# Performance work log

Measured on AMD Instinct MI355X. Metric: run time of the kernel, lower is better.

## Reference

```python
import jax, jax.numpy as jnp
import numpy as np

ALPHA = 0.2          # LeakyReLU negative slope
NEG_INF = -9e15      # mask value used by the original module


def setup_inputs() -> dict:
    key = jax.random.key(0)
    k1, k2, k3, k4 = jax.random.split(key, 4)
    N, F_IN, F_OUT = 8192, 512, 256
    inp = jax.random.normal(k1, (N, F_IN), dtype=jnp.float32)
    W = jax.random.normal(k2, (F_IN, F_OUT), dtype=jnp.float32) * (1.414 / np.sqrt(F_IN))
    a = jax.random.normal(k3, (2 * F_OUT, 1), dtype=jnp.float32) * (1.414 / np.sqrt(F_OUT))
    adj = jax.random.randint(k4, (N, N), 0, 2, dtype=jnp.int32)
    return {"input": inp, "W": W, "a": a, "adj": adj}


def reference(input, W, a, adj):
    # h: [N, F_out]
    h = input @ W
    F_out = h.shape[1]
    # Original builds a_input[i,j] = concat(h_i, h_j) then matmuls with a.
    # Equivalent: e_ij = leakyrelu(h_i . a[:F] + h_j . a[F:]) without the O(N^2 * 2F) tensor.
    a1 = a[:F_out, 0]   # [F_out]
    a2 = a[F_out:, 0]   # [F_out]
    s1 = h @ a1         # [N]
    s2 = h @ a2         # [N]
    e = jax.nn.leaky_relu(s1[:, None] + s2[None, :], negative_slope=ALPHA)  # [N, N]
    attention = jax.nn.softmax(jnp.where(adj > 0, e, NEG_INF), axis=1)       # [N, N]
    return attention @ h  # [N, F_out]
```

## Files before the change

kernel.cpp:

```cpp
#include <hip/hip_runtime.h>


typedef __attribute__((ext_vector_type(8))) short bf16x8;
typedef __attribute__((ext_vector_type(4))) float fx4;
typedef __attribute__((ext_vector_type(4))) int ix4;
typedef __attribute__((ext_vector_type(2))) unsigned int ux2;

#define NN 8192
#define FIN 512
#define FOUT 256
#define PS 136
#define AROWS 32

__device__ __forceinline__ unsigned short f2bf(float f) {
    unsigned int x = __float_as_uint(f);
    x += 0x7fffu + ((x >> 16) & 1u);
    return (unsigned short)(x >> 16);
}
__device__ __forceinline__ bf16x8 pack8(fx4 a, fx4 b) {
    bf16x8 r;
    r[0] = (short)f2bf(a[0]); r[1] = (short)f2bf(a[1]);
    r[2] = (short)f2bf(a[2]); r[3] = (short)f2bf(a[3]);
    r[4] = (short)f2bf(b[0]); r[5] = (short)f2bf(b[1]);
    r[6] = (short)f2bf(b[2]); r[7] = (short)f2bf(b[3]);
    return r;
}

__global__ void wt_kernel(const float* __restrict__ W,
                          unsigned short* __restrict__ WTt) {
    const int c = threadIdx.x;
    const int k = blockIdx.x;
    WTt[((size_t)(k >> 5) * 256 + c) * 32 + (k & 31)] = f2bf(W[k * FOUT + c]);
}

__global__ __launch_bounds__(256) void prep_kernel(
    const float* __restrict__ X,
    const unsigned short* __restrict__ WTt,
    const float* __restrict__ A,
    unsigned short* __restrict__ hTt,
    float* __restrict__ s1, float* __restrict__ s2)
{
    __shared__ float s1sh[4][16], s2sh[4][16];
    const int tid = threadIdx.x;

    const int w = tid >> 6, l = tid & 63, q = l >> 4, lr = l & 15;
    const int r0 = blockIdx.x * 16;
    const int cbase = w * 64;
    fx4 acc[4] = {};

    for (int kb = 0; kb < FIN; kb += 32) {
        const float* xp = X + (size_t)(r0 + lr) * FIN + kb + q * 8;
        bf16x8 a0 = pack8(*(const fx4*)xp, *(const fx4*)(xp + 4));
#pragma unroll
        for (int tc = 0; tc < 4; ++tc) {
            bf16x8 b = *(const bf16x8*)(WTt + ((size_t)(kb >> 5) * 256 + cbase + tc * 16 + lr) * 32 + q * 8);
            acc[tc] = __builtin_amdgcn_mfma_f32_16x16x32_bf16(a0, b, acc[tc], 0, 0, 0);
        }
    }

    const int jb = r0 >> 5, jo = (r0 & 31) + q * 4;
#pragma unroll
    for (int tc = 0; tc < 4; ++tc) {
        const int c = cbase + tc * 16 + lr;
        ux2 hp;
        hp.x = (unsigned)f2bf(acc[tc][0]) | ((unsigned)f2bf(acc[tc][1]) << 16);
        hp.y = (unsigned)f2bf(acc[tc][2]) | ((unsigned)f2bf(acc[tc][3]) << 16);
        *(ux2*)(hTt + ((size_t)jb * 256 + c) * 32 + jo) = hp;
    }

    float p1[4] = {}, p2[4] = {};
#pragma unroll
    for (int tc = 0; tc < 4; ++tc) {
        const int c = cbase + tc * 16 + lr;
        const float a1v = A[c], a2v = A[FOUT + c];
#pragma unroll
        for (int r = 0; r < 4; ++r) {
            p1[r] += acc[tc][r] * a1v;
            p2[r] += acc[tc][r] * a2v;
        }
    }
#pragma unroll
    for (int r = 0; r < 4; ++r) {
#pragma unroll
        for (int off = 1; off < 16; off <<= 1) {
            p1[r] += __shfl_xor(p1[r], off);
            p2[r] += __shfl_xor(p2[r], off);
        }
        if (lr == 0) { s1sh[w][q * 4 + r] = p1[r]; s2sh[w][q * 4 + r] = p2[r]; }
    }
    __syncthreads();
    if (tid < 16) {
        s1[r0 + tid] = s1sh[0][tid] + s1sh[1][tid] + s1sh[2][tid] + s1sh[3][tid];
        s2[r0 + tid] = s2sh[0][tid] + s2sh[1][tid] + s2sh[2][tid] + s2sh[3][tid];
    }
}

__global__ __launch_bounds__(512) void attn_kernel(
    const int* __restrict__ adj,
    const unsigned short* __restrict__ hTt,
    const float* __restrict__ s1,
    const float* __restrict__ s2,
    float* __restrict__ out)
{
    __shared__ unsigned short P[2][AROWS * PS];
    __shared__ float dsh[AROWS];

    const int tid = threadIdx.x;
    const int r0 = blockIdx.x * AROWS;

    const int prow = tid >> 4;
    const int pq = tid & 15;
    const float s1v = s1[r0 + prow];
    const int* arow = adj + (size_t)(r0 + prow) * NN + pq * 8;
    float denp = 0.f;

    const int w = tid >> 6, l = tid & 63, q = l >> 4, lr = l & 15;
    const int cbase = w * 32;
    fx4 acc[2][2] = {};

    struct LSet { ix4 v0, v1; fx4 s2a, s2b; };
    LSet LA, LB;
    bf16x8 B0[4][2], B1[4][2];

    auto loadP = [&](int kt, LSet& L) {
        const int* ap = arow + kt * 128;
        L.v0 = __builtin_nontemporal_load((const ix4*)ap);
        L.v1 = __builtin_nontemporal_load((const ix4*)(ap + 4));
        L.s2a = *(const fx4*)(s2 + kt * 128 + pq * 8);
        L.s2b = *(const fx4*)(s2 + kt * 128 + pq * 8 + 4);
    };
    auto calcP = [&](int b, const LSet& L) {
        bf16x8 pv;
#pragma unroll
        for (int j = 0; j < 8; ++j) {
            const int aj = (j < 4) ? L.v0[j] : L.v1[j - 4];
            const float s2j = (j < 4) ? L.s2a[j] : L.s2b[j - 4];
            float t = s1v + s2j;
            float e = fmaxf(t, 0.2f * t);
            e = fminf(e, 30.f);
            const float p = (aj != 0) ? __expf(e) : 0.f;
            denp += p;
            pv[j] = (short)f2bf(p);
        }
        *(bf16x8*)(&P[b][prow * PS + pq * 8]) = pv;
    };
    auto loadB = [&](int it, bf16x8 (&B)[4][2]) {
#pragma unroll
        for (int ks = 0; ks < 4; ++ks)
#pragma unroll
            for (int tc = 0; tc < 2; ++tc)
                B[ks][tc] = *(const bf16x8*)(hTt + ((size_t)(it * 4 + ks) * 256 + cbase + tc * 16 + lr) * 32 + q * 8);
    };

    auto ldsBarrier = [&]() {
        asm volatile("s_waitcnt lgkmcnt(0)" ::: "memory");
        __builtin_amdgcn_s_barrier();
    };

    const int ITERS = NN / 128;
    loadP(0, LA);
    calcP(0, LA);
    loadP(1, LA);
    loadB(0, B0);
    ldsBarrier();

    auto body = [&](int it, bf16x8 (&Bc)[4][2], bf16x8 (&Bn)[4][2],
                    LSet& Lc, LSet& Ln) {
        if (it + 1 < ITERS) loadB(it + 1, Bn);
        if (it + 2 < ITERS) loadP(it + 2, Ln);
        const unsigned short* Pb = P[it & 1];
        bf16x8 af0[4], af1[4];
#pragma unroll
        for (int ks = 0; ks < 4; ++ks) {
            af0[ks] = *(const bf16x8*)(Pb + lr * PS + ks * 32 + q * 8);
            af1[ks] = *(const bf16x8*)(Pb + (16 + lr) * PS + ks * 32 + q * 8);
        }
        __builtin_amdgcn_s_setprio(1);
#pragma unroll
        for (int ks = 0; ks < 4; ++ks)
#pragma unroll
            for (int tc = 0; tc < 2; ++tc) {
                acc[0][tc] = __builtin_amdgcn_mfma_f32_16x16x32_bf16(af0[ks], Bc[ks][tc], acc[0][tc], 0, 0, 0);
                acc[1][tc] = __builtin_amdgcn_mfma_f32_16x16x32_bf16(af1[ks], Bc[ks][tc], acc[1][tc], 0, 0, 0);
            }
        __builtin_amdgcn_s_setprio(0);
        if (it + 1 < ITERS) calcP((it + 1) & 1, Lc);
        ldsBarrier();
    };

    for (int it = 0; it < ITERS; it += 2) {
        body(it, B0, B1, LA, LB);
        body(it + 1, B1, B0, LB, LA);
    }

    float v = denp;
    v += __shfl_xor(v, 1);
    v += __shfl_xor(v, 2);
    v += __shfl_xor(v, 4);
    v += __shfl_xor(v, 8);
    if (pq == 0) dsh[prow] = v;
    __syncthreads();

#pragma unroll
    for (int mg = 0; mg < 2; ++mg) {
#pragma unroll
        for (int r = 0; r < 4; ++r) {
            const int row = mg * 16 + q * 4 + r;
            const float dinv = 1.0f / fmaxf(dsh[row], 1e-30f);
#pragma unroll
            for (int tc = 0; tc < 2; ++tc) {
                out[(size_t)(r0 + row) * FOUT + cbase + tc * 16 + lr] = acc[mg][tc][r] * dinv;
            }
        }
    }
}

extern "C" void kernel_launch(void* const* d_in, const int* in_sizes, int n_in,
                              void* d_out, int out_size, void* d_ws, size_t ws_size,
                              hipStream_t stream) {
    const float *X = nullptr, *W = nullptr, *A = nullptr;
    const int* adj = nullptr;
    for (int i = 0; i < n_in; ++i) {
        switch (in_sizes[i]) {
            case NN * FIN:   X = (const float*)d_in[i]; break;
            case FIN * FOUT: W = (const float*)d_in[i]; break;
            case 2 * FOUT:   A = (const float*)d_in[i]; break;
            case NN * NN:    adj = (const int*)d_in[i]; break;
        }
    }
    if (!X) X = (const float*)d_in[0];
    if (!W) W = (const float*)d_in[1];
    if (!A) A = (const float*)d_in[2];
    if (!adj) adj = (const int*)d_in[3];
    float* out = (float*)d_out;

    char* ws = (char*)d_ws;
    float* s1 = (float*)ws;
    float* s2 = (float*)(ws + 32768);
    unsigned short* WTt = (unsigned short*)(ws + 98304);
    unsigned short* hTt = (unsigned short*)(ws + 360448);

    wt_kernel<<<512, 256, 0, stream>>>(W, WTt);
    prep_kernel<<<512, 256, 0, stream>>>(X, WTt, A, hTt, s1, s2);
    attn_kernel<<<NN / AROWS, 512, 0, stream>>>(adj, hTt, s1, s2, out);
}
```

Measured before the change: 442.4 us.

## Retile attention kernel to 64 rows by 128 columns per block

The attention kernel now gives each block 64 rows and half of the output columns, with two blocks sharing each row group. Each thread builds twice as many probability entries per tile, using two load sets. This halves the h operand traffic per block and gives each wave a 32-row by 32-column MFMA tile. In exchange, every adjacency row is read and every exponential is computed by both column-half blocks, doubling that work unless the cache absorbs the repeated reads.

```diff
diff --git a/kernel.cpp b/kernel.cpp
--- a/kernel.cpp
+++ b/kernel.cpp
@@ -10,7 +10,7 @@
 #define FIN 512
 #define FOUT 256
 #define PS 136
-#define AROWS 32
+#define AROWS 64
 
 __device__ __forceinline__ unsigned short f2bf(float f) {
     unsigned int x = __float_as_uint(f);
@@ -106,30 +106,34 @@
     __shared__ float dsh[AROWS];
 
     const int tid = threadIdx.x;
-    const int r0 = blockIdx.x * AROWS;
-
-    const int prow = tid >> 4;
-    const int pq = tid & 15;
+    const int rg = blockIdx.x >> 1;
+    const int ch = blockIdx.x & 1;
+    const int r0 = rg * AROWS;
+    const int c0 = ch * 128;
+
+    const int prow = tid >> 3;
+    const int pq = tid & 7;
     const float s1v = s1[r0 + prow];
     const int* arow = adj + (size_t)(r0 + prow) * NN + pq * 8;
     float denp = 0.f;
 
     const int w = tid >> 6, l = tid & 63, q = l >> 4, lr = l & 15;
-    const int cbase = w * 32;
+    const int rgw = (w >> 2) * 32;
+    const int cbase = c0 + (w & 3) * 32;
     fx4 acc[2][2] = {};
 
     struct LSet { ix4 v0, v1; fx4 s2a, s2b; };
-    LSet LA, LB;
+    LSet SA, SB;
     bf16x8 B0[4][2], B1[4][2];
 
-    auto loadP = [&](int kt, LSet& L) {
-        const int* ap = arow + kt * 128;
+    auto loadS = [&](int kt, int kq, LSet& L) {
+        const int* ap = arow + kt * 128 + kq * 64;
         L.v0 = __builtin_nontemporal_load((const ix4*)ap);
         L.v1 = __builtin_nontemporal_load((const ix4*)(ap + 4));
-        L.s2a = *(const fx4*)(s2 + kt * 128 + pq * 8);
-        L.s2b = *(const fx4*)(s2 + kt * 128 + pq * 8 + 4);
-    };
-    auto calcP = [&](int b, const LSet& L) {
+        L.s2a = *(const fx4*)(s2 + kt * 128 + kq * 64 + pq * 8);
+        L.s2b = *(const fx4*)(s2 + kt * 128 + kq * 64 + pq * 8 + 4);
+    };
+    auto calcP = [&](int b, int kq, const LSet& L) {
         bf16x8 pv;
 #pragma unroll
         for (int j = 0; j < 8; ++j) {
@@ -142,7 +146,7 @@
             denp += p;
             pv[j] = (short)f2bf(p);
         }
-        *(bf16x8*)(&P[b][prow * PS + pq * 8]) = pv;
+        *(bf16x8*)(&P[b][prow * PS + kq * 64 + pq * 8]) = pv;
     };
     auto loadB = [&](int it, bf16x8 (&B)[4][2]) {
 #pragma unroll
@@ -158,22 +162,20 @@
     };
 
     const int ITERS = NN / 128;
-    loadP(0, LA);
-    calcP(0, LA);
-    loadP(1, LA);
+    loadS(0, 0, SA); loadS(0, 1, SB);
+    calcP(0, 0, SA); calcP(0, 1, SB);
+    loadS(1, 0, SA); loadS(1, 1, SB);
     loadB(0, B0);
     ldsBarrier();
 
-    auto body = [&](int it, bf16x8 (&Bc)[4][2], bf16x8 (&Bn)[4][2],
-                    LSet& Lc, LSet& Ln) {
+    auto body = [&](int it, bf16x8 (&Bc)[4][2], bf16x8 (&Bn)[4][2]) {
         if (it + 1 < ITERS) loadB(it + 1, Bn);
-        if (it + 2 < ITERS) loadP(it + 2, Ln);
         const unsigned short* Pb = P[it & 1];
         bf16x8 af0[4], af1[4];
 #pragma unroll
         for (int ks = 0; ks < 4; ++ks) {
-            af0[ks] = *(const bf16x8*)(Pb + lr * PS + ks * 32 + q * 8);
-            af1[ks] = *(const bf16x8*)(Pb + (16 + lr) * PS + ks * 32 + q * 8);
+            af0[ks] = *(const bf16x8*)(Pb + (rgw + lr) * PS + ks * 32 + q * 8);
+            af1[ks] = *(const bf16x8*)(Pb + (rgw + 16 + lr) * PS + ks * 32 + q * 8);
         }
         __builtin_amdgcn_s_setprio(1);
 #pragma unroll
@@ -184,20 +186,26 @@
                 acc[1][tc] = __builtin_amdgcn_mfma_f32_16x16x32_bf16(af1[ks], Bc[ks][tc], acc[1][tc], 0, 0, 0);
             }
         __builtin_amdgcn_s_setprio(0);
-        if (it + 1 < ITERS) calcP((it + 1) & 1, Lc);
+        if (it + 1 < ITERS) {
+            calcP((it + 1) & 1, 0, SA);
+            calcP((it + 1) & 1, 1, SB);
+        }
+        if (it + 2 < ITERS) {
+            loadS(it + 2, 0, SA);
+            loadS(it + 2, 1, SB);
+        }
         ldsBarrier();
     };
 
     for (int it = 0; it < ITERS; it += 2) {
-        body(it, B0, B1, LA, LB);
-        body(it + 1, B1, B0, LB, LA);
+        body(it, B0, B1);
+        body(it + 1, B1, B0);
     }
 
     float v = denp;
     v += __shfl_xor(v, 1);
     v += __shfl_xor(v, 2);
     v += __shfl_xor(v, 4);
-    v += __shfl_xor(v, 8);
     if (pq == 0) dsh[prow] = v;
     __syncthreads();
 
@@ -205,7 +213,7 @@
     for (int mg = 0; mg < 2; ++mg) {
 #pragma unroll
         for (int r = 0; r < 4; ++r) {
-            const int row = mg * 16 + q * 4 + r;
+            const int row = rgw + mg * 16 + q * 4 + r;
             const float dinv = 1.0f / fmaxf(dsh[row], 1e-30f);
 #pragma unroll
             for (int tc = 0; tc < 2; ++tc) {
@@ -242,5 +250,5 @@
 
     wt_kernel<<<512, 256, 0, stream>>>(W, WTt);
     prep_kernel<<<512, 256, 0, stream>>>(X, WTt, A, hTt, s1, s2);
-    attn_kernel<<<NN / AROWS, 512, 0, stream>>>(adj, hTt, s1, s2, out);
-}
+    attn_kernel<<<(NN / AROWS) * 2, 512, 0, stream>>>(adj, hTt, s1, s2, out);
+}
```

Result: slower. 475.1 us (+7.4%).
